# Kernel optimization log

Measured on AMD Instinct MI355X. Metric: run time of the kernel, lower is better.

The kernel has to match this reference:

```python
import jax, jax.numpy as jnp
import numpy as np

SUB_NO = 64
SYN_BASIS_NO = 3
T_HIST = 200
T_DATA = 100000


def setup_inputs() -> dict:
    key = jax.random.key(0)
    ks = jax.random.split(key, 5)
    # strictly-lower-triangular adjacency: each subunit integrates from ancestors
    C_den = jnp.tril((jax.random.uniform(ks[0], (SUB_NO, SUB_NO)) < 0.15).astype(jnp.float32), k=-1)
    S_conv = jax.random.normal(ks[1], (T_DATA, SUB_NO), dtype=jnp.float32)
    Y_ancest = 0.1 * jax.random.normal(ks[2], (T_DATA, SUB_NO), dtype=jnp.float32)
    # sparse binary spike trains
    Z_ancest = (jax.random.uniform(ks[3], (T_DATA, SUB_NO)) < 0.05).astype(jnp.float32)
    V_o = jnp.full((1,), -69.0, dtype=jnp.float32)
    W_sub = jnp.full((SUB_NO,), 0.25, dtype=jnp.float32)
    theta_syn = jnp.zeros((SUB_NO,), dtype=jnp.float32)
    K_spike = jnp.full((SUB_NO, SYN_BASIS_NO), 0.01, dtype=jnp.float32)
    tau_spike = jnp.arange(1.6, 1.6 + SYN_BASIS_NO, dtype=jnp.float32)
    delta_spike = jnp.zeros((SUB_NO,), dtype=jnp.float32)
    return {"S_conv": S_conv, "Y_ancest": Y_ancest, "Z_ancest": Z_ancest,
            "C_den": C_den, "V_o": V_o, "W_sub": W_sub, "theta_syn": theta_syn,
            "K_spike": K_spike, "tau_spike": tau_spike, "delta_spike": delta_spike,
            "T_hist": T_HIST}


def _ancest_kernel(K_spike, tau_spike, delta_spike, T_hist):
    # t[s, k] = max(k - delta_s, 0); kern[s, k] = sum_b (t/tau_b) exp(-t/tau_b) K[s,b]
    t = jnp.arange(T_hist, dtype=jnp.float32)[None, :] - delta_spike[:, None]
    t = jnp.maximum(t, 0.0)                                  # [sub, T_hist]
    tau = jnp.exp(tau_spike)                                 # [basis]
    t_tau = t[:, None, :] / tau[None, :, None]               # [sub, basis, T_hist]
    kern = jnp.sum(t_tau * jnp.exp(-t_tau) * K_spike[:, :, None], axis=1)
    return kern                                              # [sub, T_hist]


def reference(S_conv, Y_ancest, Z_ancest, C_den, V_o, W_sub, theta_syn,
              K_spike, tau_spike, delta_spike, T_hist):
    T_data, sub_no = S_conv.shape
    kern = _ancest_kernel(K_spike, tau_spike, delta_spike, T_hist)
    kern_f = jnp.flip(kern, axis=1)                          # matches torch.flip

    # spike_ancest[t, s, k] = sum_j C_den[s,j] Z_pad[t+k, j]  ->  precontract once
    Zc = Z_ancest @ C_den.T                                  # [T, sub]
    Zc_pad = jnp.concatenate([jnp.zeros((T_hist, sub_no), Zc.dtype), Zc], axis=0)
    # depthwise VALID conv over time: filtered[t, s] = sum_k kern_f[s,k] Zc_pad[t+k, s]
    out = jax.lax.conv_general_dilated(
        Zc_pad.T[None],                                      # [1, sub, T+T_hist]
        kern_f[:, None, :],                                  # [sub, 1, T_hist]
        window_strides=(1,), padding='VALID',
        feature_group_count=sub_no,
        dimension_numbers=('NCH', 'OIH', 'NCH'))
    filtered = out[0, :, :T_data].T                          # [T, sub]

    raw = Y_ancest @ C_den.T                                 # [T, sub]
    X_in = S_conv + theta_syn + filtered + raw
    final_Y = jax.nn.sigmoid(X_in) * W_sub + V_o
    return final_Y
```

## Files before the change

### kernel.cpp

```cpp
#include <hip/hip_runtime.h>

#define SUBS  64
#define GUARD 256
#define NCH   34
#define WU    224
#define RW    48
#define RB    (RW * 4)
#define LSTR  136

typedef _Float16 f16x8 __attribute__((ext_vector_type(8)));
typedef float    f32x4 __attribute__((ext_vector_type(4)));

__device__ inline f16x8 ld_frag(const float* p) {
    float4 a = *(const float4*)p;
    float4 b = *(const float4*)(p + 4);
    f16x8 f;
    f[0]=(_Float16)a.x; f[1]=(_Float16)a.y; f[2]=(_Float16)a.z; f[3]=(_Float16)a.w;
    f[4]=(_Float16)b.x; f[5]=(_Float16)b.y; f[6]=(_Float16)b.z; f[7]=(_Float16)b.w;
    return f;
}
__device__ inline uint pkh2(float a, float b) {
    union { _Float16 h[2]; uint u; } p;
    p.h[0] = (_Float16)a; p.h[1] = (_Float16)b; return p.u;
}

__global__ __launch_bounds__(256, 4) void k_mm(
    const float* __restrict__ Z, const float* __restrict__ Y,
    const float* __restrict__ C,
    _Float16* __restrict__ Zt, _Float16* __restrict__ Yt, int T, int rgz)
{
    __shared__ _Float16 ztl[SUBS * LSTR];
    __shared__ _Float16 ytl[SUBS * LSTR];
    const int tid  = threadIdx.x;
    const int lane = tid & 63;
    const int wv   = tid >> 6;
    const int lr   = lane & 15;
    const int lg   = lane >> 4;
    const int t0b  = blockIdx.x * 128;

    if (blockIdx.x < 8) {
        const int tile = blockIdx.x * 4 + (tid >> 6);
        uint4 z4 = {0, 0, 0, 0};
        ((uint4*)Zt)[(size_t)tile * 64 + (tid & 63)] = z4;
        ((uint4*)Yt)[(size_t)tile * 64 + (tid & 63)] = z4;
    } else if (blockIdx.x < 18) {
        const int tile = rgz + (blockIdx.x - 8) * 4 + (tid >> 6);
        uint4 z4 = {0, 0, 0, 0};
        ((uint4*)Zt)[(size_t)tile * 64 + (tid & 63)] = z4;
        ((uint4*)Yt)[(size_t)tile * 64 + (tid & 63)] = z4;
    }

    f16x8 bfr[4][2];
    #pragma unroll
    for (int nt = 0; nt < 4; ++nt)
        #pragma unroll
        for (int ks = 0; ks < 2; ++ks)
            bfr[nt][ks] = ld_frag(&C[(lr + 16 * nt) * 64 + ks * 32 + lg * 8]);

    #pragma unroll
    for (int g = 0; g < 2; ++g) {
        const int t0 = t0b + wv * 32 + g * 16;
        const int rowA = t0 + lr;
        const bool okA = rowA < T;
        f16x8 az[2], ay[2];
        #pragma unroll
        for (int ks = 0; ks < 2; ++ks) {
            if (okA) {
                az[ks] = ld_frag(&Z[(size_t)rowA * 64 + ks * 32 + lg * 8]);
                ay[ks] = ld_frag(&Y[(size_t)rowA * 64 + ks * 32 + lg * 8]);
            } else {
                az[ks] = (f16x8)(_Float16)0.f;
                ay[ks] = (f16x8)(_Float16)0.f;
            }
        }

        f32x4 accZ[4], accY[4];
        #pragma unroll
        for (int nt = 0; nt < 4; ++nt) { accZ[nt] = (f32x4){0,0,0,0}; accY[nt] = (f32x4){0,0,0,0}; }
        #pragma unroll
        for (int nt = 0; nt < 4; ++nt) {
            #pragma unroll
            for (int ks = 0; ks < 2; ++ks) {
                accZ[nt] = __builtin_amdgcn_mfma_f32_16x16x32_f16(az[ks], bfr[nt][ks], accZ[nt], 0, 0, 0);
                accY[nt] = __builtin_amdgcn_mfma_f32_16x16x32_f16(ay[ks], bfr[nt][ks], accY[nt], 0, 0, 0);
            }
        }

        #pragma unroll
        for (int nt = 0; nt < 4; ++nt) {
            const int sc = lr + 16 * nt;
            const int lt = wv * 32 + g * 16 + lg * 4;
            uint2 pz, py;
            pz.x = pkh2(accZ[nt][0], accZ[nt][1]);
            pz.y = pkh2(accZ[nt][2], accZ[nt][3]);
            py.x = pkh2(accY[nt][0], accY[nt][1]);
            py.y = pkh2(accY[nt][2], accY[nt][3]);
            *(uint2*)&ztl[sc * LSTR + lt] = pz;
            *(uint2*)&ytl[sc * LSTR + lt] = py;
        }
    }

    __syncthreads();

    const int gbase = (GUARD >> 3) + blockIdx.x * 16;
    #pragma unroll
    for (int it = 0; it < 4; ++it) {
        const int chunk = it * 256 + tid;
        const int row = chunk & 63;
        const int col = chunk >> 6;
        const int tb  = t0b + col * 8;
        if (tb + 7 < T) {
            ((uint4*)Zt)[(size_t)(gbase + col) * 64 + row] =
                *(const uint4*)&ztl[row * LSTR + col * 8];
            ((uint4*)Yt)[(size_t)(gbase + col) * 64 + row] =
                *(const uint4*)&ytl[row * LSTR + col * 8];
        } else {
            #pragma unroll
            for (int h = 0; h < 8; ++h)
                if (tb + h < T) {
                    Zt[(size_t)(gbase + col) * 512 + row * 8 + h] = ztl[row * LSTR + col * 8 + h];
                    Yt[(size_t)(gbase + col) * 512 + row * 8 + h] = ytl[row * LSTR + col * 8 + h];
                }
        }
    }
}

#define STEP3(u)                                                                 \
    _Pragma("unroll")                                                            \
    for (int b = 0; b < 3; ++b) {                                                \
        const float yn = fmaf(twr[b], y1[b], fmaf(mr2[b], y2[b], cr[b] * (u)));  \
        y2[b] = y1[b]; y1[b] = yn;                                               \
    }

#define PAIRW(wrd) {                                                             \
    union { uint u; _Float16 h[2]; } w_; w_.u = (wrd);                           \
    STEP3((float)w_.h[0]);                                                       \
    STEP3((float)w_.h[1]); }

#define CHUNK8F(cur, nxt) {                                                      \
    PAIRW((cur).w); PAIRW((nxt).x); PAIRW((nxt).y); PAIRW((nxt).z); }

__global__ __launch_bounds__(256, 3) void k_iir(
    const _Float16* __restrict__ Zt, const _Float16* __restrict__ Yt,
    const float* __restrict__ S,
    const float* __restrict__ K_spike, const float* __restrict__ tau_spike,
    const float* __restrict__ delta_spike, const float* __restrict__ theta,
    const float* __restrict__ W, const float* __restrict__ Vo,
    float* __restrict__ out, int T)
{
    const int tid = threadIdx.x;
    const int s   = tid & 63;
    const int wv  = tid >> 6;
    const int t0  = blockIdx.x * RB + wv * RW;
    if (t0 >= T) return;

    float twr[3], mr2[3], cr[3];
    #pragma unroll
    for (int b = 0; b < 3; ++b) {
        const float tau = __expf(tau_spike[b]);
        const float r   = __expf(-1.0f / tau);
        twr[b] = 2.0f * r;
        mr2[b] = -r * r;
        cr[b]  = K_spike[s * 3 + b] / tau * r;
    }
    int dl = (int)rintf(delta_spike[s]);
    dl = min(max(dl, 0), 30);
    const float th   = theta[s];
    const float wsub = W[s];
    const float vo   = Vo[0];

    float y1[3] = {0.f, 0.f, 0.f}, y2[3] = {0.f, 0.f, 0.f};

    if (__all(dl == 0)) {
        const int tile0 = (GUARD + t0 - 232) >> 3;
        const uint4* xb = (const uint4*)Zt + (size_t)tile0 * 64 + s;

        uint4 buf[8];
        #pragma unroll
        for (int p = 0; p < 8; ++p) buf[p] = xb[(size_t)p * 64];

        #pragma unroll 1
        for (int cc = 0; cc < 3; ++cc) {
            #pragma unroll
            for (int j = 0; j < 8; ++j) {
                const int c = cc * 8 + j;
                const uint4 cur = buf[j];
                const uint4 nxt = buf[(j + 1) & 7];
                buf[j] = xb[(size_t)(c + 8) * 64];
                __builtin_amdgcn_sched_barrier(0);
                CHUNK8F(cur, nxt);
            }
        }

        uint4 t32 = xb[(size_t)32 * 64];
        uint4 t33 = xb[(size_t)33 * 64];
        uint4 t34 = xb[(size_t)34 * 64];
        const uint4* yb = (const uint4*)Yt + (size_t)((GUARD + t0) >> 3) * 64 + s;
        uint4 yv[6];
        #pragma unroll
        for (int p = 0; p < 6; ++p) yv[p] = yb[(size_t)p * 64];
        uint spk[24];
        #pragma unroll
        for (int p = 0; p < 24; ++p) {
            const int t1 = min(t0 + 2 * p,     T - 1);
            const int t2 = min(t0 + 2 * p + 1, T - 1);
            spk[p] = pkh2(S[(size_t)t1 * 64 + s] + th, S[(size_t)t2 * 64 + s] + th);
        }

        #pragma unroll
        for (int j = 0; j < 4; ++j) { CHUNK8F(buf[j], buf[j + 1]); }

        #pragma unroll
        for (int oc = 0; oc < 6; ++oc) {
            uint4 cur, nxt;
            if      (oc == 0) { cur = buf[4]; nxt = buf[5]; }
            else if (oc == 1) { cur = buf[5]; nxt = buf[6]; }
            else if (oc == 2) { cur = buf[6]; nxt = buf[7]; }
            else if (oc == 3) { cur = buf[7]; nxt = t32;    }
            else if (oc == 4) { cur = t32;    nxt = t33;    }
            else              { cur = t33;    nxt = t34;    }
            const uint sw[4] = { cur.w, nxt.x, nxt.y, nxt.z };
            union { uint4 v; _Float16 h[8]; } yw; yw.v = yv[oc];
            #pragma unroll
            for (int i = 0; i < 4; ++i) {
                union { uint u; _Float16 h[2]; } w; w.u = sw[i];
                #pragma unroll
                for (int hh = 0; hh < 2; ++hh) {
                    STEP3((float)w.h[hh]);
                    const int o = oc * 8 + i * 2 + hh;
                    const int t = t0 + o;
                    if (t < T) {
                        union { uint u; _Float16 h[2]; } sp; sp.u = spk[o >> 1];
                        const float xin = (float)yw.h[i * 2 + hh] + (float)sp.h[o & 1]
                                          + y1[0] + y1[1] + y1[2];
                        const float sig = 1.0f / (1.0f + __expf(-xin));
                        out[(size_t)t * 64 + s] = fmaf(sig, wsub, vo);
                    }
                }
            }
        }
    } else {
        const int xi0 = t0 - 226 - dl;
        for (int k = 0; k < 8 * NCH; ++k) {
            const int h = GUARD + xi0 + k;
            const float u = (float)Zt[(size_t)(h >> 3) * 512 + s * 8 + (h & 7)];
            STEP3(u);
            const int o = k - WU;
            if (o >= 0) {
                const int t = t0 + o;
                if (t < T) {
                    const int hy = GUARD + t;
                    const float yc = (float)Yt[(size_t)(hy >> 3) * 512 + s * 8 + (hy & 7)];
                    const float xin = yc + S[(size_t)t * 64 + s] + th
                                      + y1[0] + y1[1] + y1[2];
                    const float sig = 1.0f / (1.0f + __expf(-xin));
                    out[(size_t)t * 64 + s] = fmaf(sig, wsub, vo);
                }
            }
        }
    }
}

extern "C" void kernel_launch(void* const* d_in, const int* in_sizes, int n_in,
                              void* d_out, int out_size, void* d_ws, size_t ws_size,
                              hipStream_t stream)
{
    const float* S     = (const float*)d_in[0];
    const float* Y     = (const float*)d_in[1];
    const float* Z     = (const float*)d_in[2];
    const float* C     = (const float*)d_in[3];
    const float* Vo    = (const float*)d_in[4];
    const float* W     = (const float*)d_in[5];
    const float* theta = (const float*)d_in[6];
    const float* K     = (const float*)d_in[7];
    const float* tau   = (const float*)d_in[8];
    const float* delta = (const float*)d_in[9];
    const int T = in_sizes[0] / SUBS;

    const int rgz    = (GUARD + T + 7) >> 3;
    const int ntiles = rgz + 44;
    _Float16* Zt = (_Float16*)d_ws;
    _Float16* Yt = (_Float16*)((char*)d_ws + (size_t)ntiles * 1024);

    k_mm<<<(T + 127) / 128, 256, 0, stream>>>(Z, Y, C, Zt, Yt, T, rgz);
    k_iir<<<(T + RB - 1) / RB, 256, 0, stream>>>(Zt, Yt, S, K, tau, delta, theta,
                                                 W, Vo, (float*)d_out, T);
}
```

Before: 56.31 us.

## Replace IIR warmup recomputation with blockwise state scan via jump matrices

Before, each wave re-ran the 3-basis second-order recurrence over about 224 warmup samples to produce 48 outputs. Now a separate k_state kernel computes each 32-step block's local final state from zero initial conditions and writes it to workspace. The main kernel then rebuilds its incoming state by combining the previous seven blocks' states with closed-form 32-step transition coefficients, and runs only its own 32 steps. This removes most of the redundant recurrence work, at the cost of an extra kernel launch and a workspace round-trip, with a truncated history window similar to before.

```diff
diff --git a/kernel.cpp b/kernel.cpp
--- a/kernel.cpp
+++ b/kernel.cpp
@@ -2,10 +2,8 @@
 
 #define SUBS  64
 #define GUARD 256
-#define NCH   34
-#define WU    224
-#define RW    48
-#define RB    (RW * 4)
+#define LB    32
+#define JT    8
 #define LSTR  136
 
 typedef _Float16 f16x8 __attribute__((ext_vector_type(8)));
@@ -137,22 +135,22 @@
     STEP3((float)w_.h[0]);                                                       \
     STEP3((float)w_.h[1]); }
 
-#define CHUNK8F(cur, nxt) {                                                      \
-    PAIRW((cur).w); PAIRW((nxt).x); PAIRW((nxt).y); PAIRW((nxt).z); }
-
-__global__ __launch_bounds__(256, 3) void k_iir(
-    const _Float16* __restrict__ Zt, const _Float16* __restrict__ Yt,
-    const float* __restrict__ S,
+__global__ __launch_bounds__(256, 4) void k_state(
+    const _Float16* __restrict__ Zt,
     const float* __restrict__ K_spike, const float* __restrict__ tau_spike,
-    const float* __restrict__ delta_spike, const float* __restrict__ theta,
-    const float* __restrict__ W, const float* __restrict__ Vo,
-    float* __restrict__ out, int T)
+    float* __restrict__ fb, int NB)
 {
     const int tid = threadIdx.x;
     const int s   = tid & 63;
     const int wv  = tid >> 6;
-    const int t0  = blockIdx.x * RB + wv * RW;
-    if (t0 >= T) return;
+    const int gi  = blockIdx.x * 4 + wv - JT;
+    if (gi >= NB) return;
+    float* fout = fb + (size_t)(gi + JT) * 384;
+    if (gi < 0) {
+        #pragma unroll
+        for (int c = 0; c < 6; ++c) fout[c * 64 + s] = 0.f;
+        return;
+    }
 
     float twr[3], mr2[3], cr[3];
     #pragma unroll
@@ -163,89 +161,143 @@
         mr2[b] = -r * r;
         cr[b]  = K_spike[s * 3 + b] / tau * r;
     }
+
+    const uint4* xb = (const uint4*)Zt + (size_t)(31 + 4 * gi) * 64 + s;
+    const uint4 x0 = xb[0];
+    const uint4 x1 = xb[64];
+    const uint4 x2 = xb[128];
+    const uint4 x3 = xb[192];
+    const uint4 x4 = xb[256];
+
+    float y1[3] = {0.f, 0.f, 0.f}, y2[3] = {0.f, 0.f, 0.f};
+    PAIRW(x0.w);
+    PAIRW(x1.x); PAIRW(x1.y); PAIRW(x1.z); PAIRW(x1.w);
+    PAIRW(x2.x); PAIRW(x2.y); PAIRW(x2.z); PAIRW(x2.w);
+    PAIRW(x3.x); PAIRW(x3.y); PAIRW(x3.z); PAIRW(x3.w);
+    PAIRW(x4.x); PAIRW(x4.y); PAIRW(x4.z);
+
+    #pragma unroll
+    for (int b = 0; b < 3; ++b) {
+        fout[(2 * b)     * 64 + s] = y1[b];
+        fout[(2 * b + 1) * 64 + s] = y2[b];
+    }
+}
+
+__global__ __launch_bounds__(256, 3) void k_iir2(
+    const _Float16* __restrict__ Zt, const _Float16* __restrict__ Yt,
+    const float* __restrict__ S,
+    const float* __restrict__ K_spike, const float* __restrict__ tau_spike,
+    const float* __restrict__ delta_spike, const float* __restrict__ theta,
+    const float* __restrict__ W, const float* __restrict__ Vo,
+    const float* __restrict__ fb, float* __restrict__ out, int T, int NB)
+{
+    const int tid = threadIdx.x;
+    const int s   = tid & 63;
+    const int wv  = tid >> 6;
+    const int i   = blockIdx.x * 4 + wv;
+    if (i >= NB) return;
+    const int t0 = i * LB;
+
+    float twr[3], mr2[3], cr[3], taus[3];
+    #pragma unroll
+    for (int b = 0; b < 3; ++b) {
+        const float tau = __expf(tau_spike[b]);
+        taus[b] = tau;
+        const float r = __expf(-1.0f / tau);
+        twr[b] = 2.0f * r;
+        mr2[b] = -r * r;
+        cr[b]  = K_spike[s * 3 + b] / tau * r;
+    }
     int dl = (int)rintf(delta_spike[s]);
     dl = min(max(dl, 0), 30);
     const float th   = theta[s];
     const float wsub = W[s];
     const float vo   = Vo[0];
 
-    float y1[3] = {0.f, 0.f, 0.f}, y2[3] = {0.f, 0.f, 0.f};
+    float y1[3], y2[3];
 
     if (__all(dl == 0)) {
-        const int tile0 = (GUARD + t0 - 232) >> 3;
-        const uint4* xb = (const uint4*)Zt + (size_t)tile0 * 64 + s;
-
-        uint4 buf[8];
-        #pragma unroll
-        for (int p = 0; p < 8; ++p) buf[p] = xb[(size_t)p * 64];
-
-        #pragma unroll 1
-        for (int cc = 0; cc < 3; ++cc) {
-            #pragma unroll
-            for (int j = 0; j < 8; ++j) {
-                const int c = cc * 8 + j;
-                const uint4 cur = buf[j];
-                const uint4 nxt = buf[(j + 1) & 7];
-                buf[j] = xb[(size_t)(c + 8) * 64];
-                __builtin_amdgcn_sched_barrier(0);
-                CHUNK8F(cur, nxt);
-            }
-        }
-
-        uint4 t32 = xb[(size_t)32 * 64];
-        uint4 t33 = xb[(size_t)33 * 64];
-        uint4 t34 = xb[(size_t)34 * 64];
-        const uint4* yb = (const uint4*)Yt + (size_t)((GUARD + t0) >> 3) * 64 + s;
-        uint4 yv[6];
-        #pragma unroll
-        for (int p = 0; p < 6; ++p) yv[p] = yb[(size_t)p * 64];
-        uint spk[24];
-        #pragma unroll
-        for (int p = 0; p < 24; ++p) {
+        float aL[3], bL[3], cL[3], dL[3];
+        #pragma unroll
+        for (int b = 0; b < 3; ++b) {
+            const float r   = 0.5f * twr[b];
+            const float rm1 = __expf(-(float)(LB - 1) / taus[b]);
+            const float rl  = rm1 * r;
+            const float rp  = rl * r;
+            aL[b] = (float)(LB + 1) * rl;
+            bL[b] = -(float)LB * rp;
+            cL[b] = (float)LB * rm1;
+            dL[b] = -(float)(LB - 1) * rl;
+        }
+        {
+            const float* fq = fb + (size_t)i * 384;
+            #pragma unroll
+            for (int b = 0; b < 3; ++b) {
+                y1[b] = fq[(2 * b) * 64 + s];
+                y2[b] = fq[(2 * b + 1) * 64 + s];
+            }
+        }
+        #pragma unroll
+        for (int j = 7; j >= 1; --j) {
+            const float* fq = fb + (size_t)(i + JT - j) * 384;
+            #pragma unroll
+            for (int b = 0; b < 3; ++b) {
+                const float f1 = fq[(2 * b) * 64 + s];
+                const float f2 = fq[(2 * b + 1) * 64 + s];
+                const float n1 = fmaf(aL[b], y1[b], fmaf(bL[b], y2[b], f1));
+                const float n2 = fmaf(cL[b], y1[b], fmaf(dL[b], y2[b], f2));
+                y1[b] = n1; y2[b] = n2;
+            }
+        }
+
+        const uint4* xb = (const uint4*)Zt + (size_t)(31 + 4 * i) * 64 + s;
+        const uint4 x0 = xb[0];
+        const uint4 x1 = xb[64];
+        const uint4 x2 = xb[128];
+        const uint4 x3 = xb[192];
+        const uint4 x4 = xb[256];
+        const uint4* yb = (const uint4*)Yt + (size_t)(32 + 4 * i) * 64 + s;
+        const uint4 yv0 = yb[0], yv1 = yb[64], yv2 = yb[128], yv3 = yb[192];
+
+        uint spk[16];
+        #pragma unroll
+        for (int p = 0; p < 16; ++p) {
             const int t1 = min(t0 + 2 * p,     T - 1);
             const int t2 = min(t0 + 2 * p + 1, T - 1);
             spk[p] = pkh2(S[(size_t)t1 * 64 + s] + th, S[(size_t)t2 * 64 + s] + th);
         }
 
-        #pragma unroll
-        for (int j = 0; j < 4; ++j) { CHUNK8F(buf[j], buf[j + 1]); }
-
-        #pragma unroll
-        for (int oc = 0; oc < 6; ++oc) {
-            uint4 cur, nxt;
-            if      (oc == 0) { cur = buf[4]; nxt = buf[5]; }
-            else if (oc == 1) { cur = buf[5]; nxt = buf[6]; }
-            else if (oc == 2) { cur = buf[6]; nxt = buf[7]; }
-            else if (oc == 3) { cur = buf[7]; nxt = t32;    }
-            else if (oc == 4) { cur = t32;    nxt = t33;    }
-            else              { cur = t33;    nxt = t34;    }
-            const uint sw[4] = { cur.w, nxt.x, nxt.y, nxt.z };
-            union { uint4 v; _Float16 h[8]; } yw; yw.v = yv[oc];
-            #pragma unroll
-            for (int i = 0; i < 4; ++i) {
-                union { uint u; _Float16 h[2]; } w; w.u = sw[i];
-                #pragma unroll
-                for (int hh = 0; hh < 2; ++hh) {
-                    STEP3((float)w.h[hh]);
-                    const int o = oc * 8 + i * 2 + hh;
-                    const int t = t0 + o;
-                    if (t < T) {
-                        union { uint u; _Float16 h[2]; } sp; sp.u = spk[o >> 1];
-                        const float xin = (float)yw.h[i * 2 + hh] + (float)sp.h[o & 1]
-                                          + y1[0] + y1[1] + y1[2];
-                        const float sig = 1.0f / (1.0f + __expf(-xin));
-                        out[(size_t)t * 64 + s] = fmaf(sig, wsub, vo);
-                    }
+        uint xw[16] = { x0.w, x1.x, x1.y, x1.z, x1.w, x2.x, x2.y, x2.z,
+                        x2.w, x3.x, x3.y, x3.z, x3.w, x4.x, x4.y, x4.z };
+        uint yw[16] = { yv0.x, yv0.y, yv0.z, yv0.w, yv1.x, yv1.y, yv1.z, yv1.w,
+                        yv2.x, yv2.y, yv2.z, yv2.w, yv3.x, yv3.y, yv3.z, yv3.w };
+
+        #pragma unroll
+        for (int w = 0; w < 16; ++w) {
+            union { uint u; _Float16 h[2]; } wx; wx.u = xw[w];
+            union { uint u; _Float16 h[2]; } wy; wy.u = yw[w];
+            union { uint u; _Float16 h[2]; } wp; wp.u = spk[w];
+            #pragma unroll
+            for (int hh = 0; hh < 2; ++hh) {
+                STEP3((float)wx.h[hh]);
+                const int t = t0 + 2 * w + hh;
+                if (t < T) {
+                    const float xin = (float)wy.h[hh] + (float)wp.h[hh]
+                                      + y1[0] + y1[1] + y1[2];
+                    const float sig = 1.0f / (1.0f + __expf(-xin));
+                    out[(size_t)t * 64 + s] = fmaf(sig, wsub, vo);
                 }
             }
         }
     } else {
+        y1[0] = y1[1] = y1[2] = 0.f;
+        y2[0] = y2[1] = y2[2] = 0.f;
         const int xi0 = t0 - 226 - dl;
-        for (int k = 0; k < 8 * NCH; ++k) {
+        for (int k = 0; k < 224 + LB; ++k) {
             const int h = GUARD + xi0 + k;
             const float u = (float)Zt[(size_t)(h >> 3) * 512 + s * 8 + (h & 7)];
             STEP3(u);
-            const int o = k - WU;
+            const int o = k - 224;
             if (o >= 0) {
                 const int t = t0 + o;
                 if (t < T) {
@@ -275,14 +327,17 @@
     const float* K     = (const float*)d_in[7];
     const float* tau   = (const float*)d_in[8];
     const float* delta = (const float*)d_in[9];
-    const int T = in_sizes[0] / SUBS;
+    const int T  = in_sizes[0] / SUBS;
+    const int NB = (T + LB - 1) / LB;
 
     const int rgz    = (GUARD + T + 7) >> 3;
     const int ntiles = rgz + 44;
     _Float16* Zt = (_Float16*)d_ws;
     _Float16* Yt = (_Float16*)((char*)d_ws + (size_t)ntiles * 1024);
+    float*    fb = (float*)((char*)d_ws + (size_t)ntiles * 2048);
 
     k_mm<<<(T + 127) / 128, 256, 0, stream>>>(Z, Y, C, Zt, Yt, T, rgz);
-    k_iir<<<(T + RB - 1) / RB, 256, 0, stream>>>(Zt, Yt, S, K, tau, delta, theta,
-                                                 W, Vo, (float*)d_out, T);
-}
+    k_state<<<(NB + JT + 3) / 4, 256, 0, stream>>>(Zt, K, tau, fb, NB);
+    k_iir2<<<(NB + 3) / 4, 256, 0, stream>>>(Zt, Yt, S, K, tau, delta, theta,
+                                             W, Vo, fb, (float*)d_out, T, NB);
+}
```

After: 49.26 us. -12.5%, faster.
